# Performance work log

Measured on AMD Instinct MI355X. Metric: run time of the kernel, lower is better.

The kernel has to match this reference:

```python
import jax, jax.numpy as jnp
import numpy as np

N, C, H = 4096, 1024, 16
HD = C // H            # 64
DR = HD // 8           # 8 rope freqs per spatial axis


def setup_inputs() -> dict:
    key = jax.random.key(0)
    k1, k2, k3, k4, k5, k6 = jax.random.split(key, 6)
    x = jax.random.normal(k1, (N, C), dtype=jnp.float32)
    coords = jax.random.randint(k2, (N, 5), 0, 64, dtype=jnp.int32)  # [batch, t, h, w, z]
    w_qkv = jax.random.normal(k3, (3 * C, C), dtype=jnp.float32) / np.sqrt(C)
    w_out = jax.random.normal(k4, (C, C), dtype=jnp.float32) / np.sqrt(C)
    gamma_q = jnp.ones((H, HD), dtype=jnp.float32)
    gamma_k = jnp.ones((H, HD), dtype=jnp.float32)
    return {"x": x, "coords": coords, "w_qkv": w_qkv, "w_out": w_out,
            "gamma_q": gamma_q, "gamma_k": gamma_k}


def _rms_norm(t, gamma):
    # F.normalize(dim=-1) * gamma * sqrt(head_dim), computed in fp32
    t = t.astype(jnp.float32)
    nrm = jnp.linalg.norm(t, axis=-1, keepdims=True)
    return t / jnp.maximum(nrm, 1e-12) * gamma * np.float32(np.sqrt(HD))


def _rope_angles(coords):
    # freqs = 1/10000^(arange(DR)/HD); angles per axis (t,h,w,z), concat -> [N, 4*DR] = [N, HD/2]
    freqs = 1.0 / (10000.0 ** (jnp.arange(DR, dtype=jnp.float32) / HD))
    pos = coords[:, 1:].astype(jnp.float32)  # [N,4]
    ang = pos[:, :, None] * freqs[None, None, :]  # [N,4,DR]
    return ang.reshape(ang.shape[0], -1)  # [N, HD/2]


def _apply_rope(t, cos, sin):
    # t: [N,H,HD]; pairs (2i, 2i+1) rotated by angle[i]
    t2 = t.astype(jnp.float32).reshape(t.shape[0], t.shape[1], -1, 2)
    re = t2[..., 0] * cos - t2[..., 1] * sin
    im = t2[..., 0] * sin + t2[..., 1] * cos
    return jnp.stack([re, im], axis=-1).reshape(t.shape)


def reference(x, coords, w_qkv, w_out, gamma_q, gamma_k):
    n = x.shape[0]
    qkv = (x @ w_qkv.T).reshape(n, 3, H, HD)
    q, k, v = qkv[:, 0], qkv[:, 1], qkv[:, 2]  # [N,H,HD]
    q = _rms_norm(q, gamma_q)
    k = _rms_norm(k, gamma_k)
    ang = _rope_angles(coords)              # [N, HD/2]
    cos = jnp.cos(ang)[:, None, :]          # [N,1,HD/2] (broadcast over heads)
    sin = jnp.sin(ang)[:, None, :]
    q = _apply_rope(q, cos, sin)
    k = _apply_rope(k, cos, sin)
    scale = np.float32(1.0 / np.sqrt(HD))
    scores = jnp.einsum('nhd,mhd->hnm', q, k) * scale  # [H,N,N]
    attn = jax.nn.softmax(scores, axis=-1)
    out = jnp.einsum('hnm,mhd->nhd', attn, v).reshape(n, C)
    return out @ w_out.T
```

## Files before the change

kernel.cpp:

```cpp
#include <hip/hip_runtime.h>
#include <hip/hip_bf16.h>

typedef _Float16 half8 __attribute__((ext_vector_type(8)));
typedef _Float16 half4v __attribute__((ext_vector_type(4)));
typedef _Float16 half2 __attribute__((ext_vector_type(2)));
typedef float f32x4 __attribute__((ext_vector_type(4)));

constexpr int NT = 4096;
constexpr int CH = 1024;
constexpr int NH = 16;
constexpr int HD = 64;
constexpr int C3 = 3072;

#if __has_builtin(__builtin_amdgcn_exp2f)
#define EXP2(x) __builtin_amdgcn_exp2f(x)
#else
#define EXP2(x) exp2f(x)
#endif

#define GLOAD_LDS16(gp, lp) __builtin_amdgcn_global_load_lds( \
    (const __attribute__((address_space(1))) void*)(gp),      \
    (__attribute__((address_space(3))) void*)(lp), 16, 0, 0)

#define WAITCNT4 do { asm volatile("s_waitcnt vmcnt(4)" ::: "memory"); \
                      __builtin_amdgcn_sched_barrier(0); } while (0)
#define WAITCNT0 do { asm volatile("s_waitcnt vmcnt(0)" ::: "memory"); \
                      __builtin_amdgcn_sched_barrier(0); } while (0)

static __device__ inline half2 pk_f16(float a, float b) {
  auto r = __builtin_amdgcn_cvt_pkrtz(a, b);
  return *(half2*)&r;
}

__global__ __launch_bounds__(256) void cvt3_kernel(const float* __restrict__ a, int na4,
                                                   const float* __restrict__ b, int nb4,
                                                   const float* __restrict__ c, int nc4,
                                                   _Float16* __restrict__ oa,
                                                   _Float16* __restrict__ ob,
                                                   _Float16* __restrict__ oc) {
  int i = blockIdx.x * 256 + threadIdx.x;
  const float* src; _Float16* dst; int j = i;
  if (i < na4) { src = a; dst = oa; }
  else if (i < na4 + nb4) { src = b; dst = ob; j = i - na4; }
  else if (i < na4 + nb4 + nc4) { src = c; dst = oc; j = i - na4 - nb4; }
  else return;
  float4 v = ((const float4*)src)[j];
  half4v h;
  h[0] = (_Float16)v.x; h[1] = (_Float16)v.y; h[2] = (_Float16)v.z; h[3] = (_Float16)v.w;
  ((half4v*)dst)[j] = h;
}

__global__ __launch_bounds__(256) void rope_tab_kernel(const int* __restrict__ coords,
                                                       float2* __restrict__ csn) {
  int idx = blockIdx.x * 256 + threadIdx.x;
  int n = idx >> 5, j = idx & 31;
  float ang = (float)coords[n * 5 + 1 + (j >> 3)] * __expf(-(float)(j & 7) * 0.14391157f);
  csn[idx] = make_float2(cosf(ang), sinf(ang));
}

__global__ __launch_bounds__(512, 2) void gemm_qkv(const _Float16* __restrict__ A,
                                                   const _Float16* __restrict__ Bt,
                                                   const float2* __restrict__ csn,
                                                   const float* __restrict__ gq,
                                                   const float* __restrict__ gk,
                                                   _Float16* __restrict__ Qh,
                                                   _Float16* __restrict__ KF,
                                                   _Float16* __restrict__ VF) {
  __shared__ __align__(16) char smem[73728];
  auto As = (_Float16(*)[256][32])smem;
  auto Bs = (_Float16(*)[256][32])(smem + 32768);
  const int K = CH;
  const int tid = threadIdx.x;
  const int lane = tid & 63, w = tid >> 6;
  const int l15 = lane & 15, l4 = lane >> 4;
  int nwg = gridDim.x, cpx = nwg >> 3;
  int wg = (blockIdx.x & 7) * cpx + (blockIdx.x >> 3);
  const int nbx = NT / 256;
  const int bm = wg % nbx, bn = wg / nbx;
  const int m0 = bm * 256, n0 = bn * 256;
  const int wr = w >> 2, wc = w & 3;
  const int rb = w * 32;
  const int rl = lane >> 2;
  const int cb = (lane & 3) * 8;
  f32x4 acc[8][4] = {};
  auto stage = [&](int k0, int buf) {
    GLOAD_LDS16(A  + (size_t)(m0 + rb + rl) * K + k0 + cb,      &As[buf][rb][0]);
    GLOAD_LDS16(A  + (size_t)(m0 + rb + 16 + rl) * K + k0 + cb, &As[buf][rb + 16][0]);
    GLOAD_LDS16(Bt + (size_t)(n0 + rb + rl) * K + k0 + cb,      &Bs[buf][rb][0]);
    GLOAD_LDS16(Bt + (size_t)(n0 + rb + 16 + rl) * K + k0 + cb, &Bs[buf][rb + 16][0]);
  };
  auto compute = [&](int buf) {
    half8 af[8], bf[4];
#pragma unroll
    for (int mt = 0; mt < 8; ++mt) af[mt] = *(half8*)&As[buf][wr * 128 + mt * 16 + l15][l4 * 8];
#pragma unroll
    for (int nt = 0; nt < 4; ++nt) bf[nt] = *(half8*)&Bs[buf][wc * 64 + nt * 16 + l15][l4 * 8];
    __builtin_amdgcn_s_setprio(1);
#pragma unroll
    for (int mt = 0; mt < 8; ++mt)
#pragma unroll
      for (int nt = 0; nt < 4; ++nt)
        acc[mt][nt] = __builtin_amdgcn_mfma_f32_16x16x32_f16(af[mt], bf[nt], acc[mt][nt], 0, 0, 0);
    __builtin_amdgcn_s_setprio(0);
  };
  stage(0, 0);
  stage(32, 1);
  for (int k0 = 0; k0 < K - 32; k0 += 32) {
    int buf = (k0 >> 5) & 1;
    WAITCNT4;
    __builtin_amdgcn_s_barrier();
    compute(buf);
    __builtin_amdgcn_s_barrier();
    if (k0 + 64 < K) stage(k0 + 64, buf);
  }
  WAITCNT0;
  __builtin_amdgcn_s_barrier();
  compute(((K - 32) >> 5) & 1);
  __builtin_amdgcn_s_barrier();
  const int gc0 = n0 + wc * 64;
  const int sec = gc0 >> 10;
  const int h   = (gc0 & 1023) >> 6;
  _Float16* Lw = (_Float16*)(smem + w * 9216);
  float gmm[4];
  if (sec < 2) {
    const float* gm = (sec == 0) ? gq : gk;
#pragma unroll
    for (int nt = 0; nt < 4; ++nt) gmm[nt] = gm[h * 64 + nt * 16 + l15];
  }
  const float qsc = (sec == 0) ? 0.18033688f : 1.0f;
#pragma unroll
  for (int half = 0; half < 2; ++half) {
    const int K0 = m0 + wr * 128 + half * 64;
    if (sec < 2) {
#pragma unroll
      for (int mt = 0; mt < 4; ++mt)
#pragma unroll
        for (int r = 0; r < 4; ++r) {
          float ss = 0.f;
#pragma unroll
          for (int nt = 0; nt < 4; ++nt)
            ss += acc[half * 4 + mt][nt][r] * acc[half * 4 + mt][nt][r];
          ss += __shfl_xor(ss, 1); ss += __shfl_xor(ss, 2);
          ss += __shfl_xor(ss, 4); ss += __shfl_xor(ss, 8);
          float sc = 8.0f / fmaxf(sqrtf(ss), 1e-12f);
          int row = mt * 16 + l4 * 4 + r;
          int n = K0 + row;
#pragma unroll
          for (int nt = 0; nt < 4; ++nt) {
            float v = acc[half * 4 + mt][nt][r] * sc * gmm[nt];
            float2 cz = csn[n * 32 + nt * 8 + (l15 >> 1)];
            float p = __shfl_xor(v, 1);
            float o = ((l15 & 1) == 0) ? (v * cz.x - p * cz.y) : (p * cz.y + v * cz.x);
            Lw[row * 72 + nt * 16 + l15] = (_Float16)(o * qsc);
          }
        }
    } else {
#pragma unroll
      for (int mt = 0; mt < 4; ++mt)
#pragma unroll
        for (int r = 0; r < 4; ++r) {
          int row = mt * 16 + l4 * 4 + r;
#pragma unroll
          for (int nt = 0; nt < 4; ++nt)
            Lw[row * 72 + nt * 16 + l15] = (_Float16)acc[half * 4 + mt][nt][r];
        }
    }
    const int kb = K0 >> 6;
    if (sec == 0) {
#pragma unroll
      for (int i = 0; i < 8; ++i) {
        int row = i * 8 + (lane >> 3), col = (lane & 7) * 8;
        half8 vv = *(half8*)&Lw[row * 72 + col];
        *(half8*)(Qh + ((size_t)h * NT + K0 + row) * 64 + col) = vv;
      }
    } else if (sec == 1) {
      _Float16* base = KF + (size_t)h * NT * HD + (size_t)kb * 4096;
#pragma unroll
      for (int i = 0; i < 8; ++i) {
        int t = i >> 1, kk = i & 1;
        int i15 = lane & 15, ll4 = lane >> 4;
        int m = ((t >> 1) << 5) | ((i15 >> 2) << 3) | ((t & 1) << 2) | (i15 & 3);
        half8 vv = *(half8*)&Lw[m * 72 + kk * 32 + ll4 * 8];
        *(half8*)(base + (size_t)(((t * 2 + kk) * 64 + ll4 * 16 + i15) * 8)) = vv;
      }
    } else {
      _Float16* base = VF + (size_t)h * NT * HD + (size_t)kb * 4096;
#pragma unroll
      for (int i = 0; i < 8; ++i) {
        int t = i >> 1, kk = i & 1;
        int l15v = lane & 15, l4v = lane >> 4;
        half8 vv;
#pragma unroll
        for (int jj = 0; jj < 8; ++jj)
          vv[jj] = Lw[(kk * 32 + l4v * 8 + jj) * 72 + t * 16 + l15v];
        *(half8*)(base + (size_t)(((t * 2 + kk) * 64 + l4v * 16 + l15v) * 8)) = vv;
      }
    }
  }
}

template <typename OutT>
__global__ __launch_bounds__(256) void gemm_bt(const _Float16* __restrict__ A,
                                               const _Float16* __restrict__ Bt,
                                               OutT* __restrict__ Cc,
                                               int M, int Nn, int K, int nbx) {
  __shared__ _Float16 As[2][128][32];
  __shared__ _Float16 Bs[2][128][32];
  const int tid = threadIdx.x;
  const int lane = tid & 63, w = tid >> 6;
  const int l15 = lane & 15, l4 = lane >> 4;
  int nwg = gridDim.x, cpx = nwg >> 3;
  int wg = (blockIdx.x & 7) * cpx + (blockIdx.x >> 3);
  const int m0 = (wg % nbx) * 128, n0 = (wg / nbx) * 128;
  const int wr = w >> 1, wc = w & 1;
  const int rb = w * 32;
  const int rl = lane >> 2;
  const int cb = (lane & 3) * 8;
  f32x4 acc[4][4] = {};
  auto stage = [&](int k0, int buf) {
    GLOAD_LDS16(A  + (size_t)(m0 + rb + rl) * K + k0 + cb,      &As[buf][rb][0]);
    GLOAD_LDS16(A  + (size_t)(m0 + rb + 16 + rl) * K + k0 + cb, &As[buf][rb + 16][0]);
    GLOAD_LDS16(Bt + (size_t)(n0 + rb + rl) * K + k0 + cb,      &Bs[buf][rb][0]);
    GLOAD_LDS16(Bt + (size_t)(n0 + rb + 16 + rl) * K + k0 + cb, &Bs[buf][rb + 16][0]);
  };
  auto compute = [&](int buf) {
    half8 af[4], bf[4];
#pragma unroll
    for (int mt = 0; mt < 4; ++mt) af[mt] = *(half8*)&As[buf][wr * 64 + mt * 16 + l15][l4 * 8];
#pragma unroll
    for (int nt = 0; nt < 4; ++nt) bf[nt] = *(half8*)&Bs[buf][wc * 64 + nt * 16 + l15][l4 * 8];
    __builtin_amdgcn_s_setprio(1);
#pragma unroll
    for (int mt = 0; mt < 4; ++mt)
#pragma unroll
      for (int nt = 0; nt < 4; ++nt)
        acc[mt][nt] = __builtin_amdgcn_mfma_f32_16x16x32_f16(af[mt], bf[nt], acc[mt][nt], 0, 0, 0);
    __builtin_amdgcn_s_setprio(0);
  };
  stage(0, 0);
  stage(32, 1);
  for (int k0 = 0; k0 < K - 32; k0 += 32) {
    int buf = (k0 >> 5) & 1;
    WAITCNT4;
    __builtin_amdgcn_s_barrier();
    compute(buf);
    __builtin_amdgcn_s_barrier();
    if (k0 + 64 < K) stage(k0 + 64, buf);
  }
  WAITCNT0;
  __builtin_amdgcn_s_barrier();
  compute(((K - 32) >> 5) & 1);
#pragma unroll
  for (int mt = 0; mt < 4; ++mt)
#pragma unroll
    for (int nt = 0; nt < 4; ++nt)
#pragma unroll
      for (int r = 0; r < 4; ++r) {
        int row = m0 + wr * 64 + mt * 16 + l4 * 4 + r;
        int col = n0 + wc * 64 + nt * 16 + l15;
        Cc[(size_t)row * Nn + col] = (OutT)acc[mt][nt][r];
      }
}

__global__ __launch_bounds__(256, 2) void attn_kernel(const _Float16* __restrict__ Qh,
                                                      const _Float16* __restrict__ KF,
                                                      const _Float16* __restrict__ VF,
                                                      _Float16* __restrict__ Oh) {
  __shared__ _Float16 KB[4096];
  __shared__ _Float16 VB[4096];
  const int tid = threadIdx.x, lane = tid & 63, w = tid >> 6;
  const int l15 = lane & 15, l4 = lane >> 4;
  int bid = blockIdx.x;
  int s = bid >> 3;
  int h = (bid & 7) * 2 + (s >> 5);
  int n0 = (s & 31) * 128;
  half8 qf[2][2];
#pragma unroll
  for (int qb = 0; qb < 2; ++qb)
#pragma unroll
    for (int kk = 0; kk < 2; ++kk)
      qf[qb][kk] = *(const half8*)(Qh + ((size_t)h * NT + n0 + w * 32 + qb * 16 + l15) * HD + kk * 32 + l4 * 8);
  f32x4 acc[2][4] = {};
  f32x4 acc5[2] = {};
  half8 of1 = {};
  if (l15 == 0) {
#pragma unroll
    for (int jq = 0; jq < 8; ++jq) of1[jq] = (_Float16)1.0f;
  }
  const _Float16* KFh = KF + (size_t)h * NT * HD + w * 512 + lane * 8;
  const _Float16* VFh = VF + (size_t)h * NT * HD + w * 512 + lane * 8;
  union U { half8 v; half2 p[4]; };
  for (int kb = 0; kb < 64; ++kb) {
    __syncthreads();
    {
      size_t g0 = (size_t)kb * 4096;
      GLOAD_LDS16(KFh + g0,        &KB[w * 512]);
      GLOAD_LDS16(KFh + g0 + 2048, &KB[2048 + w * 512]);
      GLOAD_LDS16(VFh + g0,        &VB[w * 512]);
      GLOAD_LDS16(VFh + g0 + 2048, &VB[2048 + w * 512]);
    }
    __syncthreads();
    f32x4 sv[2][4] = {};
    __builtin_amdgcn_s_setprio(1);
#pragma unroll
    for (int t = 0; t < 4; ++t)
#pragma unroll
      for (int kk = 0; kk < 2; ++kk) {
        half8 kf = *(half8*)&KB[(t * 2 + kk) * 512 + lane * 8];
        sv[0][t] = __builtin_amdgcn_mfma_f32_16x16x32_f16(kf, qf[0][kk], sv[0][t], 0, 0, 0);
        sv[1][t] = __builtin_amdgcn_mfma_f32_16x16x32_f16(kf, qf[1][kk], sv[1][t], 0, 0, 0);
      }
    __builtin_amdgcn_s_setprio(0);
    U u[2][2];
#pragma unroll
    for (int qb = 0; qb < 2; ++qb) {
      float e[4][4];
#pragma unroll
      for (int t = 0; t < 4; ++t)
#pragma unroll
        for (int r = 0; r < 4; ++r) e[t][r] = EXP2(sv[qb][t][r]);
      u[qb][0].p[0] = pk_f16(e[0][0], e[0][1]); u[qb][0].p[1] = pk_f16(e[0][2], e[0][3]);
      u[qb][0].p[2] = pk_f16(e[1][0], e[1][1]); u[qb][0].p[3] = pk_f16(e[1][2], e[1][3]);
      u[qb][1].p[0] = pk_f16(e[2][0], e[2][1]); u[qb][1].p[1] = pk_f16(e[2][2], e[2][3]);
      u[qb][1].p[2] = pk_f16(e[3][0], e[3][1]); u[qb][1].p[3] = pk_f16(e[3][2], e[3][3]);
    }
    __builtin_amdgcn_s_setprio(1);
#pragma unroll
    for (int t = 0; t < 4; ++t)
#pragma unroll
      for (int kk = 0; kk < 2; ++kk) {
        half8 vf = *(half8*)&VB[(t * 2 + kk) * 512 + lane * 8];
        acc[0][t] = __builtin_amdgcn_mfma_f32_16x16x32_f16(u[0][kk].v, vf, acc[0][t], 0, 0, 0);
        acc[1][t] = __builtin_amdgcn_mfma_f32_16x16x32_f16(u[1][kk].v, vf, acc[1][t], 0, 0, 0);
      }
    acc5[0] = __builtin_amdgcn_mfma_f32_16x16x32_f16(u[0][0].v, of1, acc5[0], 0, 0, 0);
    acc5[0] = __builtin_amdgcn_mfma_f32_16x16x32_f16(u[0][1].v, of1, acc5[0], 0, 0, 0);
    acc5[1] = __builtin_amdgcn_mfma_f32_16x16x32_f16(u[1][0].v, of1, acc5[1], 0, 0, 0);
    acc5[1] = __builtin_amdgcn_mfma_f32_16x16x32_f16(u[1][1].v, of1, acc5[1], 0, 0, 0);
    __builtin_amdgcn_s_setprio(0);
  }
#pragma unroll
  for (int qb = 0; qb < 2; ++qb) {
    float linv[4];
#pragma unroll
    for (int r = 0; r < 4; ++r) linv[r] = 1.0f / __shfl(acc5[qb][r], lane & 48);
#pragma unroll
    for (int t = 0; t < 4; ++t)
#pragma unroll
      for (int r = 0; r < 4; ++r) {
        int row = n0 + w * 32 + qb * 16 + l4 * 4 + r;
        Oh[(size_t)row * CH + h * HD + t * 16 + l15] = (_Float16)(acc[qb][t][r] * linv[r]);
      }
  }
}

extern "C" void kernel_launch(void* const* d_in, const int* in_sizes, int n_in,
                              void* d_out, int out_size, void* d_ws, size_t ws_size,
                              hipStream_t stream) {
  const float* x      = (const float*)d_in[0];
  const int*   coords = (const int*)d_in[1];
  const float* w_qkv  = (const float*)d_in[2];
  const float* w_out  = (const float*)d_in[3];
  const float* gq     = (const float*)d_in[4];
  const float* gk     = (const float*)d_in[5];
  float* out = (float*)d_out;

  char* ws = (char*)d_ws;
  size_t off = 0;
  auto alloc = [&](size_t bytes) { char* p = ws + off; off += bytes; return p; };
  _Float16* xh   = (_Float16*)alloc((size_t)NT * CH * 2);
  _Float16* wqh  = (_Float16*)alloc((size_t)C3 * CH * 2);
  _Float16* woh  = (_Float16*)alloc((size_t)CH * CH * 2);
  float2*   csn  = (float2*)alloc((size_t)NT * 32 * 8);
  _Float16* Qh   = (_Float16*)alloc((size_t)NT * CH * 2);
  _Float16* KFh  = (_Float16*)alloc((size_t)NT * CH * 2);
  _Float16* VFh  = (_Float16*)alloc((size_t)NT * CH * 2);
  _Float16* Oh   = (_Float16*)alloc((size_t)NT * CH * 2);
  if (off > ws_size) return;

  int na4 = NT * CH / 4, nb4 = C3 * CH / 4, nc4 = CH * CH / 4;
  cvt3_kernel<<<(na4 + nb4 + nc4) / 256, 256, 0, stream>>>(x, na4, w_qkv, nb4, w_out, nc4,
                                                           xh, wqh, woh);
  rope_tab_kernel<<<NT * 32 / 256, 256, 0, stream>>>(coords, csn);
  gemm_qkv<<<(NT / 256) * (C3 / 256), 512, 0, stream>>>(xh, wqh, csn, gq, gk, Qh, KFh, VFh);
  attn_kernel<<<NH * (NT / 128), 256, 0, stream>>>(Qh, KFh, VFh, Oh);
  gemm_bt<float><<<(NT / 128) * (CH / 128), 256, 0, stream>>>(Oh, woh, out, NT, CH, CH, NT / 128);
}
```

Measured before the change: 153.7 us.

## Pre-swizzle QKV GEMM operands into MFMA fragment layout and deepen K tile

The conversion kernel now writes x and w_qkv in fp16 in a tiled, MFMA-fragment-ordered layout, so the QKV GEMM can stream contiguous 16-byte chunks straight into LDS and read fragments without strided addressing. The GEMM K step grows from 32 to 64, split into two half-stage loads with finer vmcnt waits to overlap loads and compute. The rope-table kernel is merged into the prep kernel to save a launch. The launch bound drops to one block per CU because LDS use rises, which may reduce occupancy.

```diff
diff --git a/kernel.cpp b/kernel.cpp
--- a/kernel.cpp
+++ b/kernel.cpp
@@ -22,6 +22,8 @@
     (const __attribute__((address_space(1))) void*)(gp),      \
     (__attribute__((address_space(3))) void*)(lp), 16, 0, 0)
 
+#define WAITCNT8 do { asm volatile("s_waitcnt vmcnt(8)" ::: "memory"); \
+                      __builtin_amdgcn_sched_barrier(0); } while (0)
 #define WAITCNT4 do { asm volatile("s_waitcnt vmcnt(4)" ::: "memory"); \
                       __builtin_amdgcn_sched_barrier(0); } while (0)
 #define WAITCNT0 do { asm volatile("s_waitcnt vmcnt(0)" ::: "memory"); \
@@ -32,44 +34,54 @@
   return *(half2*)&r;
 }
 
-__global__ __launch_bounds__(256) void cvt3_kernel(const float* __restrict__ a, int na4,
+__global__ __launch_bounds__(256) void prep_kernel(const float* __restrict__ a, int na4,
                                                    const float* __restrict__ b, int nb4,
                                                    const float* __restrict__ c, int nc4,
+                                                   const int* __restrict__ coords,
                                                    _Float16* __restrict__ oa,
                                                    _Float16* __restrict__ ob,
-                                                   _Float16* __restrict__ oc) {
+                                                   _Float16* __restrict__ oc,
+                                                   float2* __restrict__ csn) {
   int i = blockIdx.x * 256 + threadIdx.x;
-  const float* src; _Float16* dst; int j = i;
-  if (i < na4) { src = a; dst = oa; }
-  else if (i < na4 + nb4) { src = b; dst = ob; j = i - na4; }
-  else if (i < na4 + nb4 + nc4) { src = c; dst = oc; j = i - na4 - nb4; }
-  else return;
-  float4 v = ((const float4*)src)[j];
-  half4v h;
-  h[0] = (_Float16)v.x; h[1] = (_Float16)v.y; h[2] = (_Float16)v.z; h[3] = (_Float16)v.w;
-  ((half4v*)dst)[j] = h;
-}
-
-__global__ __launch_bounds__(256) void rope_tab_kernel(const int* __restrict__ coords,
-                                                       float2* __restrict__ csn) {
-  int idx = blockIdx.x * 256 + threadIdx.x;
-  int n = idx >> 5, j = idx & 31;
-  float ang = (float)coords[n * 5 + 1 + (j >> 3)] * __expf(-(float)(j & 7) * 0.14391157f);
-  csn[idx] = make_float2(cosf(ang), sinf(ang));
-}
-
-__global__ __launch_bounds__(512, 2) void gemm_qkv(const _Float16* __restrict__ A,
-                                                   const _Float16* __restrict__ Bt,
+  int cvt_end = na4 + nb4 + nc4;
+  if (i < na4 + nb4) {
+    const float* src; _Float16* dst; int j = i;
+    if (i < na4) { src = a; dst = oa; }
+    else { src = b; dst = ob; j = i - na4; }
+    int r = j >> 8, k = (j & 255) * 4;
+    float4 v = ((const float4*)src)[j];
+    int bt = r >> 8, rr = r & 255;
+    int kt = k >> 6, kr = k & 63;
+    int frag = ((kr >> 5) << 4) + (rr >> 4);
+    size_t flat = (((size_t)bt * 16 + kt) * 32 + frag) * 512
+                + ((((kr >> 3) & 3) * 16 + (rr & 15)) << 3) + (kr & 7);
+    half4v h;
+    h[0] = (_Float16)v.x; h[1] = (_Float16)v.y; h[2] = (_Float16)v.z; h[3] = (_Float16)v.w;
+    *(half4v*)(dst + flat) = h;
+  } else if (i < cvt_end) {
+    int j = i - na4 - nb4;
+    float4 v = ((const float4*)c)[j];
+    half4v h;
+    h[0] = (_Float16)v.x; h[1] = (_Float16)v.y; h[2] = (_Float16)v.z; h[3] = (_Float16)v.w;
+    ((half4v*)oc)[j] = h;
+  } else {
+    int idx = i - cvt_end;
+    if (idx >= NT * 32) return;
+    int n = idx >> 5, j = idx & 31;
+    float ang = (float)coords[n * 5 + 1 + (j >> 3)] * __expf(-(float)(j & 7) * 0.14391157f);
+    csn[idx] = make_float2(cosf(ang), sinf(ang));
+  }
+}
+
+__global__ __launch_bounds__(512, 1) void gemm_qkv(const _Float16* __restrict__ A2,
+                                                   const _Float16* __restrict__ B2,
                                                    const float2* __restrict__ csn,
                                                    const float* __restrict__ gq,
                                                    const float* __restrict__ gk,
                                                    _Float16* __restrict__ Qh,
                                                    _Float16* __restrict__ KF,
                                                    _Float16* __restrict__ VF) {
-  __shared__ __align__(16) char smem[73728];
-  auto As = (_Float16(*)[256][32])smem;
-  auto Bs = (_Float16(*)[256][32])(smem + 32768);
-  const int K = CH;
+  __shared__ __align__(16) _Float16 smem[65536];
   const int tid = threadIdx.x;
   const int lane = tid & 63, w = tid >> 6;
   const int l15 = lane & 15, l4 = lane >> 4;
@@ -79,48 +91,68 @@
   const int bm = wg % nbx, bn = wg / nbx;
   const int m0 = bm * 256, n0 = bn * 256;
   const int wr = w >> 2, wc = w & 3;
-  const int rb = w * 32;
-  const int rl = lane >> 2;
-  const int cb = (lane & 3) * 8;
+  const _Float16* Abase = A2 + (size_t)bm * 16 * 16384 + tid * 8;
+  const _Float16* Bbase = B2 + (size_t)bn * 16 * 16384 + tid * 8;
   f32x4 acc[8][4] = {};
-  auto stage = [&](int k0, int buf) {
-    GLOAD_LDS16(A  + (size_t)(m0 + rb + rl) * K + k0 + cb,      &As[buf][rb][0]);
-    GLOAD_LDS16(A  + (size_t)(m0 + rb + 16 + rl) * K + k0 + cb, &As[buf][rb + 16][0]);
-    GLOAD_LDS16(Bt + (size_t)(n0 + rb + rl) * K + k0 + cb,      &Bs[buf][rb][0]);
-    GLOAD_LDS16(Bt + (size_t)(n0 + rb + 16 + rl) * K + k0 + cb, &Bs[buf][rb + 16][0]);
+  auto stA = [&](int kt, int buf, int s) {
+    GLOAD_LDS16(Abase + (size_t)kt * 16384 + s * 4096, &smem[buf * 16384 + s * 4096 + w * 512]);
   };
-  auto compute = [&](int buf) {
-    half8 af[8], bf[4];
-#pragma unroll
-    for (int mt = 0; mt < 8; ++mt) af[mt] = *(half8*)&As[buf][wr * 128 + mt * 16 + l15][l4 * 8];
-#pragma unroll
-    for (int nt = 0; nt < 4; ++nt) bf[nt] = *(half8*)&Bs[buf][wc * 64 + nt * 16 + l15][l4 * 8];
-    __builtin_amdgcn_s_setprio(1);
-#pragma unroll
-    for (int mt = 0; mt < 8; ++mt)
-#pragma unroll
-      for (int nt = 0; nt < 4; ++nt)
-        acc[mt][nt] = __builtin_amdgcn_mfma_f32_16x16x32_f16(af[mt], bf[nt], acc[mt][nt], 0, 0, 0);
-    __builtin_amdgcn_s_setprio(0);
+  auto stB = [&](int kt, int buf, int s) {
+    GLOAD_LDS16(Bbase + (size_t)kt * 16384 + s * 4096, &smem[32768 + buf * 16384 + s * 4096 + w * 512]);
   };
-  stage(0, 0);
-  stage(32, 1);
-  for (int k0 = 0; k0 < K - 32; k0 += 32) {
-    int buf = (k0 >> 5) & 1;
+  auto stageA0B0 = [&](int kt, int buf) { stA(kt, buf, 0); stA(kt, buf, 1); stB(kt, buf, 0); stB(kt, buf, 1); };
+  auto stageA1B1 = [&](int kt, int buf) { stA(kt, buf, 2); stA(kt, buf, 3); stB(kt, buf, 2); stB(kt, buf, 3); };
+  auto computeKK = [&](int buf, int kk) {
+    const _Float16* Ac = &smem[buf * 16384] + lane * 8;
+    const _Float16* Bc = &smem[32768 + buf * 16384] + lane * 8;
+    half8 bf[4];
+#pragma unroll
+    for (int nt = 0; nt < 4; ++nt)
+      bf[nt] = *(half8*)(Bc + (kk * 16 + wc * 4 + nt) * 512);
+#pragma unroll
+    for (int mh = 0; mh < 2; ++mh) {
+      half8 af[4];
+#pragma unroll
+      for (int mt = 0; mt < 4; ++mt)
+        af[mt] = *(half8*)(Ac + (kk * 16 + wr * 8 + mh * 4 + mt) * 512);
+      __builtin_amdgcn_s_setprio(1);
+#pragma unroll
+      for (int mt = 0; mt < 4; ++mt)
+#pragma unroll
+        for (int nt = 0; nt < 4; ++nt)
+          acc[mh * 4 + mt][nt] = __builtin_amdgcn_mfma_f32_16x16x32_f16(
+              af[mt], bf[nt], acc[mh * 4 + mt][nt], 0, 0, 0);
+      __builtin_amdgcn_s_setprio(0);
+    }
+  };
+  stageA0B0(0, 0);
+  stageA1B1(0, 0);
+  stageA0B0(1, 1);
+  for (int kt = 0; kt < 15; ++kt) {
+    const int cur = kt & 1, nxt = cur ^ 1;
+    WAITCNT8;
+    __builtin_amdgcn_s_barrier();
+    if (kt + 1 <= 15) stageA1B1(kt + 1, nxt);
+    computeKK(cur, 0);
+    WAITCNT8;
+    __builtin_amdgcn_s_barrier();
+    computeKK(cur, 1);
+    __builtin_amdgcn_s_barrier();
+    if (kt + 2 <= 15) stageA0B0(kt + 2, cur);
+  }
+  {
     WAITCNT4;
     __builtin_amdgcn_s_barrier();
-    compute(buf);
-    __builtin_amdgcn_s_barrier();
-    if (k0 + 64 < K) stage(k0 + 64, buf);
-  }
-  WAITCNT0;
-  __builtin_amdgcn_s_barrier();
-  compute(((K - 32) >> 5) & 1);
-  __builtin_amdgcn_s_barrier();
+    computeKK(1, 0);
+    WAITCNT0;
+    __builtin_amdgcn_s_barrier();
+    computeKK(1, 1);
+    __builtin_amdgcn_s_barrier();
+  }
   const int gc0 = n0 + wc * 64;
   const int sec = gc0 >> 10;
   const int h   = (gc0 & 1023) >> 6;
-  _Float16* Lw = (_Float16*)(smem + w * 9216);
+  _Float16* Lw = (_Float16*)((char*)smem + w * 9216);
   float gmm[4];
   if (sec < 2) {
     const float* gm = (sec == 0) ? gq : gk;
@@ -379,9 +411,9 @@
   if (off > ws_size) return;
 
   int na4 = NT * CH / 4, nb4 = C3 * CH / 4, nc4 = CH * CH / 4;
-  cvt3_kernel<<<(na4 + nb4 + nc4) / 256, 256, 0, stream>>>(x, na4, w_qkv, nb4, w_out, nc4,
-                                                           xh, wqh, woh);
-  rope_tab_kernel<<<NT * 32 / 256, 256, 0, stream>>>(coords, csn);
+  int nprep = na4 + nb4 + nc4 + NT * 32;
+  prep_kernel<<<(nprep + 255) / 256, 256, 0, stream>>>(x, na4, w_qkv, nb4, w_out, nc4,
+                                                       coords, xh, wqh, woh, csn);
   gemm_qkv<<<(NT / 256) * (C3 / 256), 512, 0, stream>>>(xh, wqh, csn, gq, gk, Qh, KFh, VFh);
   attn_kernel<<<NH * (NT / 128), 256, 0, stream>>>(Qh, KFh, VFh, Oh);
   gemm_bt<float><<<(NT / 128) * (CH / 128), 256, 0, stream>>>(Oh, woh, out, NT, CH, CH, NT / 128);
```

Result: no change. 155.0 us (+0.8%).
